# Performance work log

Measured on AMD Instinct MI355X. Metric: run time of the kernel, lower is better.

Reference implementation:

```python
import jax, jax.numpy as jnp
import numpy as np

NU, NT, E, H, NL, NVOC, OUT, HID2 = 100000, 400000, 400000, 128, 3, 10000, 2, 64
EPS = 1e-5


def setup_inputs() -> dict:
    key = jax.random.key(0)
    ks = jax.random.split(key, 20)
    s = 1.0 / np.sqrt(H).astype(np.float32)
    inp = {
        "x_user": jax.random.randint(ks[0], (NU,), 0, NVOC),
        "x_txn": jax.random.randint(ks[1], (NT,), 0, NVOC),
        "ei0_src": jax.random.randint(ks[2], (E,), 0, NU),
        "ei0_dst": jax.random.randint(ks[3], (E,), 0, NT),
        "ei1_src": jax.random.randint(ks[4], (E,), 0, NT),
        "ei1_dst": jax.random.randint(ks[5], (E,), 0, NU),
        "emb_user": jax.random.normal(ks[6], (NVOC, H), jnp.float32),
        "emb_txn": jax.random.normal(ks[7], (NVOC, H), jnp.float32),
        "Wl": jax.random.normal(ks[8], (NL, 2, H, H), jnp.float32) * s,
        "bl": jax.random.normal(ks[9], (NL, 2, H), jnp.float32) * 0.01,
        "Wr": jax.random.normal(ks[10], (NL, 2, H, H), jnp.float32) * s,
        "bn_gamma": jax.random.uniform(ks[11], (NL, 2, H), jnp.float32, 0.5, 1.5),
        "bn_beta": jax.random.normal(ks[12], (NL, 2, H), jnp.float32) * 0.01,
        "bn_mean": jax.random.normal(ks[13], (NL, 2, H), jnp.float32) * 0.01,
        "bn_var": jax.random.uniform(ks[14], (NL, 2, H), jnp.float32, 0.5, 1.5),
        "W1": jax.random.normal(ks[15], (H, HID2), jnp.float32) * s,
        "b1": jax.random.normal(ks[16], (HID2,), jnp.float32) * 0.01,
        "W2": jax.random.normal(ks[17], (HID2, OUT), jnp.float32) * (1.0 / np.sqrt(HID2).astype(np.float32)),
        "b2": jax.random.normal(ks[18], (OUT,), jnp.float32) * 0.01,
    }
    return inp


def _seg_mean(src_feat, src_idx, dst_idx, num_dst):
    # gather per-edge src features, mean-reduce per dst node (SAGEConv aggr='mean')
    msg = src_feat[src_idx]                                        # [E, H]
    tot = jax.ops.segment_sum(msg, dst_idx, num_segments=num_dst)  # [Ndst, H]
    cnt = jax.ops.segment_sum(jnp.ones((dst_idx.shape[0], 1), src_feat.dtype),
                              dst_idx, num_segments=num_dst)
    return tot / jnp.maximum(cnt, 1.0)


def _bn_relu(x, g, b, m, v):
    return jax.nn.relu((x - m) * jax.lax.rsqrt(v + EPS) * g + b)


def reference(x_user, x_txn, ei0_src, ei0_dst, ei1_src, ei1_dst,
              emb_user, emb_txn, Wl, bl, Wr,
              bn_gamma, bn_beta, bn_mean, bn_var, W1, b1, W2, b2):
    h_u = emb_user[x_user]   # [NU, H]
    h_t = emb_txn[x_txn]     # [NT, H]
    for i in range(NL):
        # edge type 0: user -> transaction; edge type 1: transaction -> user
        agg_t = _seg_mean(h_u, ei0_src, ei0_dst, h_t.shape[0])
        agg_u = _seg_mean(h_t, ei1_src, ei1_dst, h_u.shape[0])
        new_t = agg_t @ Wl[i, 0] + bl[i, 0] + h_t @ Wr[i, 0]
        new_u = agg_u @ Wl[i, 1] + bl[i, 1] + h_u @ Wr[i, 1]
        h_u = _bn_relu(new_u, bn_gamma[i, 0], bn_beta[i, 0], bn_mean[i, 0], bn_var[i, 0])
        h_t = _bn_relu(new_t, bn_gamma[i, 1], bn_beta[i, 1], bn_mean[i, 1], bn_var[i, 1])
    h = jnp.concatenate([h_u, h_t], axis=0)            # [NU+NT, H]
    out = jax.nn.relu(h @ W1 + b1) @ W2 + b2           # [NU+NT, OUT]
    return out
```

## Files before the change

### kernel.cpp

```cpp
#include <hip/hip_runtime.h>


#define NUv   100000
#define NTv   400000
#define Ev    400000
#define Hv    128
#define NLv   3
#define HID2v 64
#define EPSv  1e-5f

typedef _Float16 h16;
typedef __attribute__((ext_vector_type(8))) _Float16 f16x8;
typedef __attribute__((ext_vector_type(4))) float    f32x4;

#define WS_NEED (280u * 1024u * 1024u)
__device__ __attribute__((aligned(256))) static unsigned char g_ws[WS_NEED];

__device__ __forceinline__ int imin(int a, int b) { return a < b ? a : b; }
__device__ __forceinline__ int swz(int n, int kbyte) {
  return n * 256 + (kbyte ^ ((n & 7) << 4));
}

__global__ __launch_bounds__(256) void k_count(const int* __restrict__ d0,
                                               const int* __restrict__ d1,
                                               int* __restrict__ c0,
                                               int* __restrict__ c1, int e) {
  int t = blockIdx.x * 256 + threadIdx.x;
  if (t < e) {
    atomicAdd(c0 + d0[t], 1);
    atomicAdd(c1 + d1[t], 1);
  }
}

__global__ __launch_bounds__(256) void k_blocksum(const int* __restrict__ cnt,
                                                  int* __restrict__ bs, int n) {
  __shared__ int red[256];
  int base = blockIdx.x * 2048 + threadIdx.x * 8;
  int s = 0;
#pragma unroll
  for (int j = 0; j < 8; j++) {
    int p = base + j;
    if (p < n) s += cnt[p];
  }
  red[threadIdx.x] = s;
  __syncthreads();
  for (int st = 128; st > 0; st >>= 1) {
    if (threadIdx.x < st) red[threadIdx.x] += red[threadIdx.x + st];
    __syncthreads();
  }
  if (threadIdx.x == 0) bs[blockIdx.x] = red[0];
}

__global__ __launch_bounds__(256) void k_scansmall(int* __restrict__ bs, int g) {
  __shared__ int lds[256];
  int t = threadIdx.x;
  int v = (t < g) ? bs[t] : 0;
  lds[t] = v;
  __syncthreads();
  for (int st = 1; st < 256; st <<= 1) {
    int x = (t >= st) ? lds[t - st] : 0;
    __syncthreads();
    lds[t] += x;
    __syncthreads();
  }
  if (t < g) bs[t] = lds[t] - v;
}

__global__ __launch_bounds__(256) void k_scanfinal(const int* __restrict__ cnt,
                                                   const int* __restrict__ bs,
                                                   int* __restrict__ off,
                                                   int* __restrict__ cur, int n) {
  __shared__ int lds[256];
  int t = threadIdx.x;
  int base = blockIdx.x * 2048 + t * 8;
  int v[8], pre[8];
  int tsum = 0;
#pragma unroll
  for (int j = 0; j < 8; j++) {
    int p = base + j;
    v[j] = (p < n) ? cnt[p] : 0;
    pre[j] = tsum;
    tsum += v[j];
  }
  lds[t] = tsum;
  __syncthreads();
  for (int st = 1; st < 256; st <<= 1) {
    int x = (t >= st) ? lds[t - st] : 0;
    __syncthreads();
    lds[t] += x;
    __syncthreads();
  }
  int texcl = lds[t] - tsum;
  int boff = bs[blockIdx.x];
#pragma unroll
  for (int j = 0; j < 8; j++) {
    int p = base + j;
    if (p < n) {
      int o = boff + texcl + pre[j];
      off[p] = o;
      cur[p] = o;
      if (p == n - 1) off[n] = o + v[j];
    }
  }
}

__global__ __launch_bounds__(256) void k_fill(const int* __restrict__ s0,
                                              const int* __restrict__ d0,
                                              const int* __restrict__ s1,
                                              const int* __restrict__ d1,
                                              int* __restrict__ cur0,
                                              int* __restrict__ cur1,
                                              int* __restrict__ ss0,
                                              int* __restrict__ ss1, int e) {
  int t = blockIdx.x * 256 + threadIdx.x;
  if (t < e) {
    int p = atomicAdd(cur0 + d0[t], 1);
    ss0[p] = s0[t];
    int q = atomicAdd(cur1 + d1[t], 1);
    ss1[q] = s1[t];
  }
}

__global__ __launch_bounds__(256) void k_wt(const float* __restrict__ Wl,
                                            const float* __restrict__ Wr,
                                            const float* __restrict__ W1,
                                            h16* __restrict__ WlT,
                                            h16* __restrict__ WrT,
                                            h16* __restrict__ W1T) {
  int t = blockIdx.x * 256 + threadIdx.x;
  const int NW = NLv * 2 * Hv * Hv;
  if (t < NW) {
    int mat = t / (Hv * Hv);
    int n = (t / Hv) % Hv;
    int k = t % Hv;
    WlT[t] = (h16)Wl[(size_t)mat * Hv * Hv + (size_t)k * Hv + n];
    WrT[t] = (h16)Wr[(size_t)mat * Hv * Hv + (size_t)k * Hv + n];
  } else if (t < NW + HID2v * Hv) {
    int u = t - NW;
    int n = u / Hv;
    int k = u % Hv;
    W1T[u] = (h16)W1[(size_t)k * HID2v + n];
  }
}

__global__ __launch_bounds__(256) void k_bn(const float* __restrict__ g,
                                            const float* __restrict__ b,
                                            const float* __restrict__ m,
                                            const float* __restrict__ v,
                                            float* __restrict__ sc,
                                            float* __restrict__ sh) {
  int t = blockIdx.x * 256 + threadIdx.x;
  if (t < NLv * 2 * Hv) {
    float inv = rsqrtf(v[t] + EPSv);
    float s = g[t] * inv;
    sc[t] = s;
    sh[t] = b[t] - m[t] * s;
  }
}

__global__ __launch_bounds__(256) void k_embed(const int* __restrict__ xu,
                                               const int* __restrict__ xt,
                                               const float* __restrict__ eu,
                                               const float* __restrict__ et,
                                               h16* __restrict__ hu,
                                               h16* __restrict__ ht) {
  int t = blockIdx.x * 256 + threadIdx.x;
  int row = t >> 4;
  int c = (t & 15) * 8;
  if (row >= NUv + NTv) return;
  const float* src;
  h16* dst;
  if (row < NUv) {
    src = eu + (size_t)xu[row] * Hv;
    dst = hu + (size_t)row * Hv;
  } else {
    int r2 = row - NUv;
    src = et + (size_t)xt[r2] * Hv;
    dst = ht + (size_t)r2 * Hv;
  }
  float4 v0 = *(const float4*)(src + c);
  float4 v1 = *(const float4*)(src + c + 4);
  f16x8 o;
  o[0] = (h16)v0.x; o[1] = (h16)v0.y; o[2] = (h16)v0.z; o[3] = (h16)v0.w;
  o[4] = (h16)v1.x; o[5] = (h16)v1.y; o[6] = (h16)v1.z; o[7] = (h16)v1.w;
  *(f16x8*)(dst + c) = o;
}

__global__ __launch_bounds__(512, 4) void k_fused(const h16* __restrict__ SRC,
                                                  const h16* __restrict__ DENSE,
                                                  const int* __restrict__ off,
                                                  const int* __restrict__ ss,
                                                  const h16* __restrict__ BTl,
                                                  const h16* __restrict__ BTr,
                                                  const float* __restrict__ bl,
                                                  const float* __restrict__ sc,
                                                  const float* __restrict__ sh,
                                                  h16* __restrict__ C, int M) {
  __shared__ __align__(16) unsigned char sA[128 * 256];
  __shared__ __align__(16) unsigned char sB[128 * 256];
  int t = threadIdx.x;
  int blockBase = blockIdx.x * 128;
  int w = t >> 6, l = t & 63;
  int lm = l & 15, lk = l >> 4;
  int rowBase = blockBase + w * 16;

  const h16* bsrc = BTr + t * 32;
  f16x8 br0 = *(const f16x8*)(bsrc + 0);
  f16x8 br1 = *(const f16x8*)(bsrc + 8);
  f16x8 br2 = *(const f16x8*)(bsrc + 16);
  f16x8 br3 = *(const f16x8*)(bsrc + 24);

  int ar = imin(rowBase + lm, M - 1);
  const h16* arow = DENSE + (size_t)ar * Hv;
  f16x8 ad0 = *(const f16x8*)(arow + 0 * 32 + lk * 8);
  f16x8 ad1 = *(const f16x8*)(arow + 1 * 32 + lk * 8);
  f16x8 ad2 = *(const f16x8*)(arow + 2 * 32 + lk * 8);
  f16x8 ad3 = *(const f16x8*)(arow + 3 * 32 + lk * 8);

  {
    int r = t >> 2;
    int cs = (t & 3) * 32;
    float facc[32];
#pragma unroll
    for (int j = 0; j < 32; j++) facc[j] = 0.f;
    int row = blockBase + r;
    if (row < M) {
      int e0 = off[row], e1 = off[row + 1];
      for (int e = e0; e < e1; e++) {
        const f16x8* sp = (const f16x8*)(SRC + (size_t)ss[e] * Hv + cs);
#pragma unroll
        for (int q = 0; q < 4; q++) {
          f16x8 v = sp[q];
#pragma unroll
          for (int j = 0; j < 8; j++) facc[q * 8 + j] += (float)v[j];
        }
      }
      int deg = e1 - e0;
      float inv = 1.f / (float)(deg > 1 ? deg : 1);
#pragma unroll
      for (int j = 0; j < 32; j++) facc[j] *= inv;
    }
#pragma unroll
    for (int q = 0; q < 4; q++) {
      f16x8 ov;
#pragma unroll
      for (int j = 0; j < 8; j++) ov[j] = (h16)facc[q * 8 + j];
      *(f16x8*)(sA + swz(r, cs * 2 + q * 16)) = ov;
    }
  }

  {
    int n = (t * 32) >> 7;
    int kb = ((t * 32) & 127) * 2;
    *(f16x8*)(sB + swz(n, kb + 0)) = br0;
    *(f16x8*)(sB + swz(n, kb + 16)) = br1;
    *(f16x8*)(sB + swz(n, kb + 32)) = br2;
    *(f16x8*)(sB + swz(n, kb + 48)) = br3;
  }
  __syncthreads();

  const h16* bsrc2 = BTl + t * 32;
  f16x8 bl0 = *(const f16x8*)(bsrc2 + 0);
  f16x8 bl1 = *(const f16x8*)(bsrc2 + 8);
  f16x8 bl2 = *(const f16x8*)(bsrc2 + 16);
  f16x8 bl3 = *(const f16x8*)(bsrc2 + 24);

  f32x4 acc[8];
#pragma unroll
  for (int nf = 0; nf < 8; nf++) acc[nf] = (f32x4){0.f, 0.f, 0.f, 0.f};
  {
    f16x8 ads[4] = {ad0, ad1, ad2, ad3};
#pragma unroll
    for (int s = 0; s < 4; s++) {
#pragma unroll
      for (int nf = 0; nf < 8; nf++) {
        f16x8 b = *(const f16x8*)(sB + swz(nf * 16 + lm, s * 64 + lk * 16));
        acc[nf] = __builtin_amdgcn_mfma_f32_16x16x32_f16(ads[s], b, acc[nf], 0, 0, 0);
      }
    }
  }
  __syncthreads();

  {
    int n = (t * 32) >> 7;
    int kb = ((t * 32) & 127) * 2;
    *(f16x8*)(sB + swz(n, kb + 0)) = bl0;
    *(f16x8*)(sB + swz(n, kb + 16)) = bl1;
    *(f16x8*)(sB + swz(n, kb + 32)) = bl2;
    *(f16x8*)(sB + swz(n, kb + 48)) = bl3;
  }
  __syncthreads();

#pragma unroll
  for (int s = 0; s < 4; s++) {
    f16x8 a = *(const f16x8*)(sA + swz(w * 16 + lm, s * 64 + lk * 16));
#pragma unroll
    for (int nf = 0; nf < 8; nf++) {
      f16x8 b = *(const f16x8*)(sB + swz(nf * 16 + lm, s * 64 + lk * 16));
      acc[nf] = __builtin_amdgcn_mfma_f32_16x16x32_f16(a, b, acc[nf], 0, 0, 0);
    }
  }
  __syncthreads();

#pragma unroll
  for (int nf = 0; nf < 8; nf++) {
    int col = nf * 16 + lm;
    float blv = bl[col], scv = sc[col], shv = sh[col];
#pragma unroll
    for (int r_ = 0; r_ < 4; r_++) {
      float x = fmaf(acc[nf][r_] + blv, scv, shv);
      h16 hv = (h16)fmaxf(x, 0.f);
      int rowl = w * 16 + lk * 4 + r_;
      *(h16*)(sA + swz(rowl, col * 2)) = hv;
    }
  }
  __syncthreads();
  {
    int r = t >> 2, cs = (t & 3) * 32;
    int row = blockBase + r;
    if (row < M) {
#pragma unroll
      for (int q = 0; q < 4; q++) {
        f16x8 v = *(const f16x8*)(sA + swz(r, cs * 2 + q * 16));
        *(f16x8*)(C + (size_t)row * Hv + cs + q * 8) = v;
      }
    }
  }
}

__global__ __launch_bounds__(512, 4) void k_mlp(const h16* __restrict__ HU,
                                                const h16* __restrict__ HT,
                                                const h16* __restrict__ W1T,
                                                const float* __restrict__ b1,
                                                const float* __restrict__ W2,
                                                const float* __restrict__ b2,
                                                float* __restrict__ out, int Mtot) {
  __shared__ float y[128][65];
  __shared__ __align__(16) unsigned char sW[64 * 256];
  int t = threadIdx.x;
  int w = t >> 6, l = t & 63;
  int lm = l & 15, lk = l >> 4;

  {
    const h16* src = W1T + t * 16;
    f16x8 w0 = *(const f16x8*)(src + 0);
    f16x8 w1 = *(const f16x8*)(src + 8);
    int n = (t * 16) >> 7;
    int kb = ((t * 16) & 127) * 2;
    *(f16x8*)(sW + swz(n, kb + 0)) = w0;
    *(f16x8*)(sW + swz(n, kb + 16)) = w1;
  }

  int rowBase = blockIdx.x * 128 + w * 16;
  int ar = imin(rowBase + lm, Mtot - 1);
  const h16* arow =
      (ar < NUv) ? (HU + (size_t)ar * Hv) : (HT + (size_t)(ar - NUv) * Hv);
  f16x8 a0 = *(const f16x8*)(arow + 0 * 32 + lk * 8);
  f16x8 a1 = *(const f16x8*)(arow + 1 * 32 + lk * 8);
  f16x8 a2 = *(const f16x8*)(arow + 2 * 32 + lk * 8);
  f16x8 a3 = *(const f16x8*)(arow + 3 * 32 + lk * 8);
  __syncthreads();

  f32x4 acc[4];
#pragma unroll
  for (int nf = 0; nf < 4; nf++) acc[nf] = (f32x4){0.f, 0.f, 0.f, 0.f};
  {
    f16x8 as[4] = {a0, a1, a2, a3};
#pragma unroll
    for (int s = 0; s < 4; s++) {
#pragma unroll
      for (int nf = 0; nf < 4; nf++) {
        f16x8 b = *(const f16x8*)(sW + swz(nf * 16 + lm, s * 64 + lk * 16));
        acc[nf] = __builtin_amdgcn_mfma_f32_16x16x32_f16(as[s], b, acc[nf], 0, 0, 0);
      }
    }
  }
#pragma unroll
  for (int nf = 0; nf < 4; nf++) {
    int col = nf * 16 + lm;
    float b1v = b1[col];
#pragma unroll
    for (int r = 0; r < 4; r++) {
      int rloc = w * 16 + lk * 4 + r;
      y[rloc][col] = fmaxf(acc[nf][r] + b1v, 0.f);
    }
  }
  __syncthreads();
  if (t < 256) {
    int rloc = t >> 1, o = t & 1;
    int row = blockIdx.x * 128 + rloc;
    if (row < Mtot) {
      float sum = b2[o];
#pragma unroll
      for (int k = 0; k < HID2v; k++) sum += y[rloc][k] * W2[k * 2 + o];
      out[(size_t)row * 2 + o] = sum;
    }
  }
}

extern "C" void kernel_launch(void* const* d_in, const int* in_sizes, int n_in,
                              void* d_out, int out_size, void* d_ws, size_t ws_size,
                              hipStream_t stream) {
  (void)in_sizes; (void)n_in; (void)out_size;

  const int* x_user  = (const int*)d_in[0];
  const int* x_txn   = (const int*)d_in[1];
  const int* ei0_src = (const int*)d_in[2];
  const int* ei0_dst = (const int*)d_in[3];
  const int* ei1_src = (const int*)d_in[4];
  const int* ei1_dst = (const int*)d_in[5];
  const float* emb_user = (const float*)d_in[6];
  const float* emb_txn  = (const float*)d_in[7];
  const float* Wl = (const float*)d_in[8];
  const float* bl = (const float*)d_in[9];
  const float* Wr = (const float*)d_in[10];
  const float* bn_g = (const float*)d_in[11];
  const float* bn_b = (const float*)d_in[12];
  const float* bn_m = (const float*)d_in[13];
  const float* bn_v = (const float*)d_in[14];
  const float* W1 = (const float*)d_in[15];
  const float* b1 = (const float*)d_in[16];
  const float* W2 = (const float*)d_in[17];
  const float* b2 = (const float*)d_in[18];
  float* out = (float*)d_out;

  char* wsb;
  if (ws_size >= (size_t)WS_NEED) {
    wsb = (char*)d_ws;
  } else {
    void* sym = nullptr;
    hipGetSymbolAddress(&sym, HIP_SYMBOL(g_ws));
    wsb = (char*)sym;
  }
  size_t o = 0;
  auto alloc = [&](size_t bytes) -> void* {
    o = (o + 255) & ~(size_t)255;
    void* p = wsb + o;
    o += bytes;
    return p;
  };
  h16* hu   = (h16*)alloc((size_t)NUv * Hv * 2);
  h16* ht0  = (h16*)alloc((size_t)NTv * Hv * 2);
  h16* ht1  = (h16*)alloc((size_t)NTv * Hv * 2);
  h16* WlT  = (h16*)alloc((size_t)NLv * 2 * Hv * Hv * 2);
  h16* WrT  = (h16*)alloc((size_t)NLv * 2 * Hv * Hv * 2);
  h16* W1T  = (h16*)alloc((size_t)HID2v * Hv * 2);
  float* bnsc = (float*)alloc((size_t)NLv * 2 * Hv * 4);
  float* bnsh = (float*)alloc((size_t)NLv * 2 * Hv * 4);
  int* off0 = (int*)alloc((size_t)(NTv + 1) * 4);
  int* off1 = (int*)alloc((size_t)(NUv + 1) * 4);
  int* cur0 = (int*)alloc((size_t)NTv * 4);
  int* cur1 = (int*)alloc((size_t)NUv * 4);
  int* ss0  = (int*)alloc((size_t)Ev * 4);
  int* ss1  = (int*)alloc((size_t)Ev * 4);
  int* bs0  = (int*)alloc(256 * 4);
  int* bs1  = (int*)alloc(256 * 4);

  const int G_E    = (Ev + 255) / 256;
  const int G_BS0  = (NTv + 2047) / 2048;
  const int G_BS1  = (NUv + 2047) / 2048;
  const int G_EMB  = ((NUv + NTv) * 16 + 255) / 256;
  const int G_WT   = (NLv * 2 * Hv * Hv + HID2v * Hv + 255) / 256;
  const int G_T    = (NTv + 127) / 128;
  const int G_U    = (NUv + 127) / 128;
  const int G_MLP  = (NUv + NTv + 127) / 128;

  hipMemsetAsync(cur0, 0, (size_t)NTv * 4, stream);
  hipMemsetAsync(cur1, 0, (size_t)NUv * 4, stream);
  k_count<<<G_E, 256, 0, stream>>>(ei0_dst, ei1_dst, cur0, cur1, Ev);
  k_blocksum<<<G_BS0, 256, 0, stream>>>(cur0, bs0, NTv);
  k_blocksum<<<G_BS1, 256, 0, stream>>>(cur1, bs1, NUv);
  k_scansmall<<<1, 256, 0, stream>>>(bs0, G_BS0);
  k_scansmall<<<1, 256, 0, stream>>>(bs1, G_BS1);
  k_scanfinal<<<G_BS0, 256, 0, stream>>>(cur0, bs0, off0, cur0, NTv);
  k_scanfinal<<<G_BS1, 256, 0, stream>>>(cur1, bs1, off1, cur1, NUv);
  k_fill<<<G_E, 256, 0, stream>>>(ei0_src, ei0_dst, ei1_src, ei1_dst,
                                  cur0, cur1, ss0, ss1, Ev);

  k_wt<<<G_WT, 256, 0, stream>>>(Wl, Wr, W1, WlT, WrT, W1T);
  k_bn<<<3, 256, 0, stream>>>(bn_g, bn_b, bn_m, bn_v, bnsc, bnsh);

  k_embed<<<G_EMB, 256, 0, stream>>>(x_user, x_txn, emb_user, emb_txn, hu, ht0);

  h16* ht_cur = ht0; h16* ht_nxt = ht1;
  for (int i = 0; i < NLv; i++) {
    const h16* WlT0 = WlT + (size_t)(i * 2 + 0) * Hv * Hv;
    const h16* WlT1 = WlT + (size_t)(i * 2 + 1) * Hv * Hv;
    const h16* WrT0 = WrT + (size_t)(i * 2 + 0) * Hv * Hv;
    const h16* WrT1 = WrT + (size_t)(i * 2 + 1) * Hv * Hv;
    const float* bl0 = bl + (size_t)(i * 2 + 0) * Hv;
    const float* bl1 = bl + (size_t)(i * 2 + 1) * Hv;
    const float* sc0 = bnsc + (size_t)(i * 2 + 0) * Hv;
    const float* sh0 = bnsh + (size_t)(i * 2 + 0) * Hv;
    const float* sc1 = bnsc + (size_t)(i * 2 + 1) * Hv;
    const float* sh1 = bnsh + (size_t)(i * 2 + 1) * Hv;

    k_fused<<<G_T, 512, 0, stream>>>(hu, ht_cur, off0, ss0, WlT0, WrT0,
                                     bl0, sc1, sh1, ht_nxt, NTv);
    k_fused<<<G_U, 512, 0, stream>>>(ht_cur, hu, off1, ss1, WlT1, WrT1,
                                     bl1, sc0, sh0, hu, NUv);
    h16* tmp = ht_cur; ht_cur = ht_nxt; ht_nxt = tmp;
  }

  k_mlp<<<G_MLP, 512, 0, stream>>>(hu, ht_cur, W1T, b1, W2, b2, out, NUv + NTv);
}
```

Before: 695.4 us.

## Halve rows per block in fused SAGE kernel and split N across wave pairs

The fused gather-mean plus dual GEMM kernel now handles 64 rows per 512-thread block instead of 128. Pairs of waves share a 16-row tile, each computing half of the 128 output columns. Each thread gathers 16 columns rather than 32, and the edge loop is unrolled by two so more loads are in flight. Smaller shared memory and register footprints target occupancy of 6 blocks per CU. The cost is a doubled grid with more redundant weight staging into shared memory per row.

```diff
diff --git a/kernel.cpp b/kernel.cpp
--- a/kernel.cpp
+++ b/kernel.cpp
@@ -186,7 +186,7 @@
   *(f16x8*)(dst + c) = o;
 }
 
-__global__ __launch_bounds__(512, 4) void k_fused(const h16* __restrict__ SRC,
+__global__ __launch_bounds__(512, 6) void k_fused(const h16* __restrict__ SRC,
                                                   const h16* __restrict__ DENSE,
                                                   const int* __restrict__ off,
                                                   const int* __restrict__ ss,
@@ -196,133 +196,141 @@
                                                   const float* __restrict__ sc,
                                                   const float* __restrict__ sh,
                                                   h16* __restrict__ C, int M) {
-  __shared__ __align__(16) unsigned char sA[128 * 256];
+  __shared__ __align__(16) unsigned char sA[64 * 256];
   __shared__ __align__(16) unsigned char sB[128 * 256];
   int t = threadIdx.x;
-  int blockBase = blockIdx.x * 128;
-  int w = t >> 6, l = t & 63;
+  int blockBase = blockIdx.x * 64;
+  int l = t & 63;
   int lm = l & 15, lk = l >> 4;
-  int rowBase = blockBase + w * 16;
-
-  const h16* bsrc = BTr + t * 32;
-  f16x8 br0 = *(const f16x8*)(bsrc + 0);
-  f16x8 br1 = *(const f16x8*)(bsrc + 8);
-  f16x8 br2 = *(const f16x8*)(bsrc + 16);
-  f16x8 br3 = *(const f16x8*)(bsrc + 24);
-
+  int rt = (t >> 6) >> 1, nh = (t >> 6) & 1;
+  int rowBase = blockBase + rt * 16;
+
+  {
+    const h16* bsrc = BTr + t * 32;
+    f16x8 b0 = *(const f16x8*)(bsrc + 0);
+    f16x8 b1 = *(const f16x8*)(bsrc + 8);
+    f16x8 b2 = *(const f16x8*)(bsrc + 16);
+    f16x8 b3 = *(const f16x8*)(bsrc + 24);
+    int n = t >> 2;
+    int kb = (t & 3) * 64;
+    *(f16x8*)(sB + swz(n, kb + 0)) = b0;
+    *(f16x8*)(sB + swz(n, kb + 16)) = b1;
+    *(f16x8*)(sB + swz(n, kb + 32)) = b2;
+    *(f16x8*)(sB + swz(n, kb + 48)) = b3;
+  }
   int ar = imin(rowBase + lm, M - 1);
   const h16* arow = DENSE + (size_t)ar * Hv;
   f16x8 ad0 = *(const f16x8*)(arow + 0 * 32 + lk * 8);
   f16x8 ad1 = *(const f16x8*)(arow + 1 * 32 + lk * 8);
   f16x8 ad2 = *(const f16x8*)(arow + 2 * 32 + lk * 8);
   f16x8 ad3 = *(const f16x8*)(arow + 3 * 32 + lk * 8);
-
-  {
-    int r = t >> 2;
-    int cs = (t & 3) * 32;
-    float facc[32];
-#pragma unroll
-    for (int j = 0; j < 32; j++) facc[j] = 0.f;
+  __syncthreads();
+
+  {
+    int r = t >> 3;
+    int cs = (t & 7) * 16;
+    float facc[16];
+#pragma unroll
+    for (int j = 0; j < 16; j++) facc[j] = 0.f;
     int row = blockBase + r;
     if (row < M) {
       int e0 = off[row], e1 = off[row + 1];
-      for (int e = e0; e < e1; e++) {
-        const f16x8* sp = (const f16x8*)(SRC + (size_t)ss[e] * Hv + cs);
-#pragma unroll
-        for (int q = 0; q < 4; q++) {
-          f16x8 v = sp[q];
-#pragma unroll
-          for (int j = 0; j < 8; j++) facc[q * 8 + j] += (float)v[j];
+      for (int e = e0; e < e1; e += 2) {
+        int i0 = ss[e];
+        bool v1 = (e + 1) < e1;
+        int i1 = v1 ? ss[e + 1] : i0;
+        const f16x8* p0 = (const f16x8*)(SRC + (size_t)i0 * Hv + cs);
+        const f16x8* p1 = (const f16x8*)(SRC + (size_t)i1 * Hv + cs);
+        f16x8 x0 = p0[0], x1 = p0[1];
+        f16x8 y0 = p1[0], y1 = p1[1];
+        float m1 = v1 ? 1.f : 0.f;
+#pragma unroll
+        for (int j = 0; j < 8; j++) {
+          facc[j] += (float)x0[j];
+          facc[8 + j] += (float)x1[j];
+          facc[j] = fmaf((float)y0[j], m1, facc[j]);
+          facc[8 + j] = fmaf((float)y1[j], m1, facc[8 + j]);
         }
       }
       int deg = e1 - e0;
       float inv = 1.f / (float)(deg > 1 ? deg : 1);
 #pragma unroll
-      for (int j = 0; j < 32; j++) facc[j] *= inv;
-    }
-#pragma unroll
-    for (int q = 0; q < 4; q++) {
+      for (int j = 0; j < 16; j++) facc[j] *= inv;
+    }
+#pragma unroll
+    for (int q = 0; q < 2; q++) {
       f16x8 ov;
 #pragma unroll
       for (int j = 0; j < 8; j++) ov[j] = (h16)facc[q * 8 + j];
-      *(f16x8*)(sA + swz(r, cs * 2 + q * 16)) = ov;
-    }
-  }
-
-  {
-    int n = (t * 32) >> 7;
-    int kb = ((t * 32) & 127) * 2;
-    *(f16x8*)(sB + swz(n, kb + 0)) = br0;
-    *(f16x8*)(sB + swz(n, kb + 16)) = br1;
-    *(f16x8*)(sB + swz(n, kb + 32)) = br2;
-    *(f16x8*)(sB + swz(n, kb + 48)) = br3;
-  }
-  __syncthreads();
-
-  const h16* bsrc2 = BTl + t * 32;
-  f16x8 bl0 = *(const f16x8*)(bsrc2 + 0);
-  f16x8 bl1 = *(const f16x8*)(bsrc2 + 8);
-  f16x8 bl2 = *(const f16x8*)(bsrc2 + 16);
-  f16x8 bl3 = *(const f16x8*)(bsrc2 + 24);
-
-  f32x4 acc[8];
-#pragma unroll
-  for (int nf = 0; nf < 8; nf++) acc[nf] = (f32x4){0.f, 0.f, 0.f, 0.f};
+      *(f16x8*)(sA + swz(r, (t & 7) * 32 + q * 16)) = ov;
+    }
+  }
+
+  f32x4 acc[4];
+#pragma unroll
+  for (int j = 0; j < 4; j++) acc[j] = (f32x4){0.f, 0.f, 0.f, 0.f};
   {
     f16x8 ads[4] = {ad0, ad1, ad2, ad3};
 #pragma unroll
     for (int s = 0; s < 4; s++) {
 #pragma unroll
-      for (int nf = 0; nf < 8; nf++) {
+      for (int j = 0; j < 4; j++) {
+        int nf = nh * 4 + j;
         f16x8 b = *(const f16x8*)(sB + swz(nf * 16 + lm, s * 64 + lk * 16));
-        acc[nf] = __builtin_amdgcn_mfma_f32_16x16x32_f16(ads[s], b, acc[nf], 0, 0, 0);
+        acc[j] = __builtin_amdgcn_mfma_f32_16x16x32_f16(ads[s], b, acc[j], 0, 0, 0);
       }
     }
   }
   __syncthreads();
 
   {
-    int n = (t * 32) >> 7;
-    int kb = ((t * 32) & 127) * 2;
-    *(f16x8*)(sB + swz(n, kb + 0)) = bl0;
-    *(f16x8*)(sB + swz(n, kb + 16)) = bl1;
-    *(f16x8*)(sB + swz(n, kb + 32)) = bl2;
-    *(f16x8*)(sB + swz(n, kb + 48)) = bl3;
+    const h16* bsrc = BTl + t * 32;
+    f16x8 b0 = *(const f16x8*)(bsrc + 0);
+    f16x8 b1 = *(const f16x8*)(bsrc + 8);
+    f16x8 b2 = *(const f16x8*)(bsrc + 16);
+    f16x8 b3 = *(const f16x8*)(bsrc + 24);
+    int n = t >> 2;
+    int kb = (t & 3) * 64;
+    *(f16x8*)(sB + swz(n, kb + 0)) = b0;
+    *(f16x8*)(sB + swz(n, kb + 16)) = b1;
+    *(f16x8*)(sB + swz(n, kb + 32)) = b2;
+    *(f16x8*)(sB + swz(n, kb + 48)) = b3;
   }
   __syncthreads();
 
 #pragma unroll
   for (int s = 0; s < 4; s++) {
-    f16x8 a = *(const f16x8*)(sA + swz(w * 16 + lm, s * 64 + lk * 16));
-#pragma unroll
-    for (int nf = 0; nf < 8; nf++) {
+    f16x8 a = *(const f16x8*)(sA + swz(rt * 16 + lm, s * 64 + lk * 16));
+#pragma unroll
+    for (int j = 0; j < 4; j++) {
+      int nf = nh * 4 + j;
       f16x8 b = *(const f16x8*)(sB + swz(nf * 16 + lm, s * 64 + lk * 16));
-      acc[nf] = __builtin_amdgcn_mfma_f32_16x16x32_f16(a, b, acc[nf], 0, 0, 0);
-    }
-  }
-  __syncthreads();
-
-#pragma unroll
-  for (int nf = 0; nf < 8; nf++) {
-    int col = nf * 16 + lm;
+      acc[j] = __builtin_amdgcn_mfma_f32_16x16x32_f16(a, b, acc[j], 0, 0, 0);
+    }
+  }
+  __syncthreads();
+
+#pragma unroll
+  for (int j = 0; j < 4; j++) {
+    int col = (nh * 4 + j) * 16 + lm;
     float blv = bl[col], scv = sc[col], shv = sh[col];
 #pragma unroll
     for (int r_ = 0; r_ < 4; r_++) {
-      float x = fmaf(acc[nf][r_] + blv, scv, shv);
+      float x = fmaf(acc[j][r_] + blv, scv, shv);
       h16 hv = (h16)fmaxf(x, 0.f);
-      int rowl = w * 16 + lk * 4 + r_;
+      int rowl = rt * 16 + lk * 4 + r_;
       *(h16*)(sA + swz(rowl, col * 2)) = hv;
     }
   }
   __syncthreads();
   {
-    int r = t >> 2, cs = (t & 3) * 32;
+    int r = t >> 3;
     int row = blockBase + r;
     if (row < M) {
 #pragma unroll
-      for (int q = 0; q < 4; q++) {
-        f16x8 v = *(const f16x8*)(sA + swz(r, cs * 2 + q * 16));
-        *(f16x8*)(C + (size_t)row * Hv + cs + q * 8) = v;
+      for (int q = 0; q < 2; q++) {
+        f16x8 v = *(const f16x8*)(sA + swz(r, (t & 7) * 32 + q * 16));
+        *(f16x8*)(C + (size_t)row * Hv + (t & 7) * 16 + q * 8) = v;
       }
     }
   }
@@ -461,8 +469,8 @@
   const int G_BS1  = (NUv + 2047) / 2048;
   const int G_EMB  = ((NUv + NTv) * 16 + 255) / 256;
   const int G_WT   = (NLv * 2 * Hv * Hv + HID2v * Hv + 255) / 256;
-  const int G_T    = (NTv + 127) / 128;
-  const int G_U    = (NUv + 127) / 128;
+  const int G_T    = (NTv + 63) / 64;
+  const int G_U    = (NUv + 63) / 64;
   const int G_MLP  = (NUv + NTv + 127) / 128;
 
   hipMemsetAsync(cur0, 0, (size_t)NTv * 4, stream);
```

Result: slower. 713.8 us (+2.6%).
